# Optimization experiments

Measured on AMD Instinct MI355X. Metric: run time of the kernel, lower is better.

The kernel has to match this reference:

```python
import jax, jax.numpy as jnp
import numpy as np

NEG_SLOPE = 0.2  # PyG GATConv default leaky_relu slope


def gat_conv(h_in, src, dst, W, a_src, a_dst, b, N):
    # h_in: [N, Fin]; src/dst: [E] (self-loops already appended)
    h = h_in @ W                      # [N, Fout]
    alpha_src = h @ a_src             # [N]
    alpha_dst = h @ a_dst             # [N]
    e = jax.nn.leaky_relu(alpha_src[src] + alpha_dst[dst], NEG_SLOPE)  # [E]
    # segment softmax over incoming edges of each destination node
    m = jax.ops.segment_max(e, dst, num_segments=N)
    m = jnp.where(jnp.isfinite(m), m, 0.0)
    p = jnp.exp(e - m[dst])
    denom = jax.ops.segment_sum(p, dst, num_segments=N)
    alpha = p / jnp.maximum(denom[dst], 1e-16)
    out = jax.ops.segment_sum(alpha[:, None] * h[src], dst, num_segments=N)
    return out + b


def setup_inputs() -> dict:
    key = jax.random.key(0)
    ks = jax.random.split(key, 16)
    N, E, V, D, H, C, G = 100000, 1600000, 128, 50, 16, 10, 512
    x = jax.random.normal(ks[0], (N, V), dtype=jnp.float32)
    edge_index = jax.random.randint(ks[1], (2, E), 0, N, dtype=jnp.int32)
    batch = jnp.sort(jax.random.randint(ks[2], (N,), 0, G, dtype=jnp.int32))
    s = lambda fan: 1.0 / np.sqrt(fan)
    return {
        "x": x, "edge_index": edge_index, "batch": batch,
        "embedding": jax.random.normal(ks[3], (V, D), dtype=jnp.float32),
        "W1": jax.random.normal(ks[4], (D, H), dtype=jnp.float32) * s(D),
        "a_src1": jax.random.normal(ks[5], (H,), dtype=jnp.float32) * s(H),
        "a_dst1": jax.random.normal(ks[6], (H,), dtype=jnp.float32) * s(H),
        "b1": jnp.zeros((H,), dtype=jnp.float32),
        "W2": jax.random.normal(ks[7], (H, H), dtype=jnp.float32) * s(H),
        "a_src2": jax.random.normal(ks[8], (H,), dtype=jnp.float32) * s(H),
        "a_dst2": jax.random.normal(ks[9], (H,), dtype=jnp.float32) * s(H),
        "b2": jnp.zeros((H,), dtype=jnp.float32),
        "W3": jax.random.normal(ks[10], (H, C), dtype=jnp.float32) * s(H),
        "a_src3": jax.random.normal(ks[11], (C,), dtype=jnp.float32) * s(C),
        "a_dst3": jax.random.normal(ks[12], (C,), dtype=jnp.float32) * s(C),
        "b3": jnp.zeros((C,), dtype=jnp.float32),
    }


def reference(x, edge_index, batch, embedding, W1, a_src1, a_dst1, b1,
              W2, a_src2, a_dst2, b2, W3, a_src3, a_dst3, b3):
    N = x.shape[0]
    G = 512  # num graphs
    # embedding lookup via argmax over one-hot-ish features
    idx = jnp.argmax(x, axis=1)
    h = embedding[idx]                               # [N, 50]
    # add self-loops once (PyG GATConv default)
    loops = jnp.arange(N, dtype=edge_index.dtype)
    src = jnp.concatenate([edge_index[0], loops])
    dst = jnp.concatenate([edge_index[1], loops])
    h = jax.nn.relu(gat_conv(h, src, dst, W1, a_src1, a_dst1, b1, N))
    # dropout: eval mode -> identity
    h = jax.nn.relu(gat_conv(h, src, dst, W2, a_src2, a_dst2, b2, N))
    h = gat_conv(h, src, dst, W3, a_src3, a_dst3, b3, N)  # [N, C]
    # global mean pool over graphs
    sums = jax.ops.segment_sum(h, batch, num_segments=G)
    cnts = jax.ops.segment_sum(jnp.ones((N,), h.dtype), batch, num_segments=G)
    pooled = sums / jnp.maximum(cnts, 1.0)[:, None]
    return jax.nn.softmax(pooled, axis=1)
```

## Files before the change

kernel.cpp:

```cpp
#include <hip/hip_runtime.h>
#include <math.h>

#define NEG_SLOPE 0.2f
#define NBUK_MAX 2048

__global__ void k_argmax(const float* __restrict__ x, int* __restrict__ idx, int N, int V) {
    int node = (blockIdx.x * blockDim.x + threadIdx.x) >> 5;
    int lane = threadIdx.x & 31;
    if (node >= N) return;
    const float4* row = (const float4*)(x + (long long)node * V);
    float bv = -INFINITY;
    int bi = 0x7fffffff;
    int nq = V >> 2;
    for (int q = lane; q < nq; q += 32) {
        float4 v = row[q];
        int base = q << 2;
        if (v.x > bv || (v.x == bv && base     < bi)) { bv = v.x; bi = base;     }
        if (v.y > bv || (v.y == bv && base + 1 < bi)) { bv = v.y; bi = base + 1; }
        if (v.z > bv || (v.z == bv && base + 2 < bi)) { bv = v.z; bi = base + 2; }
        if (v.w > bv || (v.w == bv && base + 3 < bi)) { bv = v.w; bi = base + 3; }
    }
    for (int off = 16; off > 0; off >>= 1) {
        float ov = __shfl_down(bv, off, 32);
        int   oi = __shfl_down(bi, off, 32);
        if (ov > bv || (ov == bv && oi < bi)) { bv = ov; bi = oi; }
    }
    if (lane == 0) idx[node] = bi;
}

template <int FIN, int FOUT>
__global__ void k_transform(const float* __restrict__ h_in, const int* __restrict__ idx,
                            const float* __restrict__ W,
                            const float* __restrict__ a_src, const float* __restrict__ a_dst,
                            _Float16* __restrict__ h_t, float* __restrict__ asrc,
                            float* __restrict__ adst, int N) {
    __shared__ float sW[FIN * FOUT];
    __shared__ float sa[FOUT], sd[FOUT];
    for (int i = threadIdx.x; i < FIN * FOUT; i += blockDim.x) sW[i] = W[i];
    if (threadIdx.x < FOUT) { sa[threadIdx.x] = a_src[threadIdx.x]; sd[threadIdx.x] = a_dst[threadIdx.x]; }
    __syncthreads();
    int n = blockIdx.x * blockDim.x + threadIdx.x;
    if (n >= N) return;
    float acc[FOUT];
#pragma unroll
    for (int f = 0; f < FOUT; f++) acc[f] = 0.f;
    const float* hr = h_in + (long long)idx[n] * FIN;
    for (int k = 0; k < FIN; k++) {
        float v = hr[k];
#pragma unroll
        for (int f = 0; f < FOUT; f++) acc[f] += v * sW[k * FOUT + f];
    }
    float s1 = 0.f, s2 = 0.f;
    _Float16 hh[16];
#pragma unroll
    for (int f = 0; f < 16; f++) hh[f] = (_Float16)0.f;
#pragma unroll
    for (int f = 0; f < FOUT; f++) {
        hh[f] = (_Float16)acc[f];
        s1 += acc[f] * sa[f];
        s2 += acc[f] * sd[f];
    }
    uint4* dst = (uint4*)(h_t + (long long)n * 16);
    dst[0] = ((uint4*)hh)[0];
    dst[1] = ((uint4*)hh)[1];
    asrc[n] = s1;
    adst[n] = s2;
}

template <int B2>
__global__ void __launch_bounds__(1024)
k_histB(const int* __restrict__ edst, int E, int* __restrict__ histT, int NBUK) {
    __shared__ int sh[NBUK_MAX];
    int t = threadIdx.x, b = blockIdx.x;
    for (int k = t; k < NBUK; k += 1024) sh[k] = 0;
    __syncthreads();
    long long ebeg = (long long)b * E / B2, eend = (long long)(b + 1) * E / B2;
    for (long long i = ebeg + t; i < eend; i += 1024)
        atomicAdd(&sh[edst[i] >> 6], 1);
    __syncthreads();
    for (int k = t; k < NBUK; k += 1024) histT[(long long)k * B2 + b] = sh[k];
}

__global__ void k_scan1(const int* __restrict__ vals, int* __restrict__ excl,
                        int* __restrict__ bsums, int M) {
    __shared__ int s[256];
    int i = blockIdx.x * 256 + threadIdx.x;
    int v = (i < M) ? vals[i] : 0;
    s[threadIdx.x] = v;
    __syncthreads();
    for (int off = 1; off < 256; off <<= 1) {
        int a = (threadIdx.x >= (unsigned)off) ? s[threadIdx.x - off] : 0;
        __syncthreads();
        s[threadIdx.x] += a;
        __syncthreads();
    }
    if (i < M) excl[i] = s[threadIdx.x] - v;
    if (threadIdx.x == 255) bsums[blockIdx.x] = s[255];
}

__global__ void k_scan2(int* __restrict__ bsums, int nb) {
    __shared__ int s[2048];
    int i = threadIdx.x;
    int v0 = (i < nb) ? bsums[i] : 0;
    int v1 = (i + 1024 < nb) ? bsums[i + 1024] : 0;
    s[i] = v0;
    s[i + 1024] = v1;
    __syncthreads();
    for (int off = 1; off < 2048; off <<= 1) {
        int a0 = (i >= off) ? s[i - off] : 0;
        int a1 = (i + 1024 >= off) ? s[i + 1024 - off] : 0;
        __syncthreads();
        s[i] += a0;
        s[i + 1024] += a1;
        __syncthreads();
    }
    if (i < nb) bsums[i] = s[i] - v0;
    if (i + 1024 < nb) bsums[i + 1024] = s[i + 1024] - v1;
}

template <int B2>
__global__ void __launch_bounds__(1024)
k_scatB(const int* __restrict__ esrc, const int* __restrict__ edst, int E,
        const int* __restrict__ sexcl, const int* __restrict__ bsums,
        int* __restrict__ tmp, int NBUK) {
    __shared__ int cur[NBUK_MAX];
    int t = threadIdx.x, b = blockIdx.x;
    for (int k = t; k < NBUK; k += 1024)
        cur[k] = sexcl[(long long)k * B2 + b] + bsums[k];
    __syncthreads();
    long long ebeg = (long long)b * E / B2, eend = (long long)(b + 1) * E / B2;
    for (long long i = ebeg + t; i < eend; i += 1024) {
        int d = edst[i];
        int pos = atomicAdd(&cur[d >> 6], 1);
        tmp[pos] = ((d & 63) << 18) | esrc[i];
    }
}

template <int B2>
__global__ void __launch_bounds__(256)
k_binB(const int* __restrict__ sexcl, const int* __restrict__ bsums,
       const int* __restrict__ tmp,
       int* __restrict__ rowptr, int* __restrict__ csr_src, int N, int NBUK, int E) {
    __shared__ int cnt[64];
    __shared__ int cur[64];
    int t = threadIdx.x, b = blockIdx.x;
    int t0 = sexcl[(long long)b * B2] + bsums[b];
    int t1 = (b + 1 < NBUK) ? (sexcl[(long long)(b + 1) * B2] + bsums[b + 1]) : E;
    if (t < 64) cnt[t] = 0;
    __syncthreads();
    for (int i = t0 + t; i < t1; i += 256) atomicAdd(&cnt[tmp[i] >> 18], 1);
    __syncthreads();
    if (t < 64) {
        int v = cnt[t];
        int incl = v;
        for (int off = 1; off < 64; off <<= 1) {
            int u = __shfl_up(incl, off, 64);
            if (t >= off) incl += u;
        }
        int base = t0 + incl - v;
        int d = (b << 6) + t;
        if (d < N) rowptr[d] = base;
        cur[t] = base;
        if (d == N - 1) rowptr[N] = E;
    }
    __syncthreads();
    for (int i = t0 + t; i < t1; i += 256) {
        int p = tmp[i];
        int pos = atomicAdd(&cur[p >> 18], 1);
        csr_src[pos] = p & 0x3FFFF;
    }
}

template <typename EPI>
__device__ __forceinline__ void gat_core(const int* __restrict__ rowptr,
                                         const int* __restrict__ csr_src,
                                         const float* __restrict__ asrc,
                                         const float* __restrict__ adst,
                                         const _Float16* __restrict__ h_t,
                                         int N, int grp, int lane, EPI epilogue) {
    int d = grp;
    int r0 = rowptr[d], r1 = rowptr[d + 1];
    float ad = adst[d];

    float e0 = asrc[d] + ad;
    e0 = (e0 >= 0.f) ? e0 : NEG_SLOPE * e0;
    float p0 = __expf(e0);
    float acc  = p0 * (float)h_t[(long long)d * 16 + lane];
    float psum = (lane == 0) ? p0 : 0.f;

    int j = r0;
    if (j < r1) {
        int myj = j + lane;
        bool valid = myj < r1;
        int s = valid ? csr_src[myj] : d;
        float a = asrc[s];
        while (true) {
            int jn = j + 16;
            int s2 = d; float a2 = 0.f; bool validn = false;
            if (jn < r1) {
                int myjn = jn + lane;
                validn = myjn < r1;
                s2 = validn ? csr_src[myjn] : d;
                a2 = asrc[s2];
            }
            float e = a + ad;
            e = (e >= 0.f) ? e : NEG_SLOPE * e;
            float p = valid ? __expf(e) : 0.f;
            psum += p;
#pragma unroll
            for (int k = 0; k < 16; k++) {
                float pk = __shfl(p, k, 16);
                int   sk = __shfl(s, k, 16);
                acc += pk * (float)h_t[(long long)sk * 16 + lane];
            }
            if (jn >= r1) break;
            j = jn; s = s2; a = a2; valid = validn;
        }
    }
    for (int off = 8; off > 0; off >>= 1) psum += __shfl_xor(psum, off, 16);
    epilogue(d, acc / fmaxf(psum, 1e-16f));
}

template <int FN>
__global__ void k_gat_ft(const int* __restrict__ rowptr, const int* __restrict__ csr_src,
                         const float* __restrict__ asrc, const float* __restrict__ adst,
                         const _Float16* __restrict__ h_t, const float* __restrict__ bias,
                         const float* __restrict__ Wn, const float* __restrict__ an_src,
                         const float* __restrict__ an_dst,
                         _Float16* __restrict__ h_next, float* __restrict__ asrc_n,
                         float* __restrict__ adst_n, int N) {
    __shared__ float sW[16 * FN];
    __shared__ float sa[FN], sd[FN], sb[16];
    for (int i = threadIdx.x; i < 16 * FN; i += blockDim.x) sW[i] = Wn[i];
    if (threadIdx.x < FN) { sa[threadIdx.x] = an_src[threadIdx.x]; sd[threadIdx.x] = an_dst[threadIdx.x]; }
    if (threadIdx.x < 16) sb[threadIdx.x] = bias[threadIdx.x];
    __syncthreads();

    int grp  = (blockIdx.x * blockDim.x + threadIdx.x) >> 4;
    int lane = threadIdx.x & 15;
    if (grp >= N) return;

    gat_core(rowptr, csr_src, asrc, adst, h_t, N, grp, lane,
        [&](int d, float v) {
            v = fmaxf(v + sb[lane], 0.f);
            float acc2 = 0.f;
#pragma unroll
            for (int k = 0; k < 16; k++) {
                float vk = __shfl(v, k, 16);
                if (lane < FN) acc2 += vk * sW[k * FN + lane];
            }
            float c1 = (lane < FN) ? acc2 * sa[lane] : 0.f;
            float c2 = (lane < FN) ? acc2 * sd[lane] : 0.f;
            for (int off = 8; off > 0; off >>= 1) {
                c1 += __shfl_xor(c1, off, 16);
                c2 += __shfl_xor(c2, off, 16);
            }
            h_next[(long long)d * 16 + lane] = (_Float16)((lane < FN) ? acc2 : 0.f);
            if (lane == 0) { asrc_n[d] = c1; adst_n[d] = c2; }
        });
}

template <int FOUT>
__global__ void k_gat_last(const int* __restrict__ rowptr, const int* __restrict__ csr_src,
                           const float* __restrict__ asrc, const float* __restrict__ adst,
                           const _Float16* __restrict__ h_t, float* __restrict__ out, int N) {
    int grp  = (blockIdx.x * blockDim.x + threadIdx.x) >> 4;
    int lane = threadIdx.x & 15;
    if (grp >= N) return;
    gat_core(rowptr, csr_src, asrc, adst, h_t, N, grp, lane,
        [&](int d, float v) {
            if (lane < FOUT) out[(long long)d * FOUT + lane] = v;
        });
}

__global__ void k_pool(const float* __restrict__ h3, const int* __restrict__ batch,
                       const float* __restrict__ b3, float* __restrict__ out, int N, int C) {
    int g = blockIdx.x;
    int lo = 0, hi = N;
    while (lo < hi) { int mid = (lo + hi) >> 1; if (batch[mid] < g) lo = mid + 1; else hi = mid; }
    int start = lo;
    hi = N;
    while (lo < hi) { int mid = (lo + hi) >> 1; if (batch[mid] < g + 1) lo = mid + 1; else hi = mid; }
    int end = lo;

    float sum[16];
    for (int f = 0; f < C; f++) sum[f] = 0.f;
    for (int n = start + threadIdx.x; n < end; n += blockDim.x) {
        const float* r = h3 + (long long)n * C;
        for (int f = 0; f < C; f++) sum[f] += r[f];
    }
    __shared__ float red[256 * 16];
    for (int f = 0; f < C; f++) red[threadIdx.x * 16 + f] = sum[f];
    __syncthreads();
    for (int str = blockDim.x / 2; str > 0; str >>= 1) {
        if ((int)threadIdx.x < str)
            for (int f = 0; f < C; f++) red[threadIdx.x * 16 + f] += red[(threadIdx.x + str) * 16 + f];
        __syncthreads();
    }
    if (threadIdx.x == 0) {
        float cnt = fmaxf((float)(end - start), 1.f);
        float vals[16];
        float mx = -INFINITY;
        for (int f = 0; f < C; f++) { vals[f] = red[f] / cnt + b3[f]; mx = fmaxf(mx, vals[f]); }
        float se = 0.f;
        for (int f = 0; f < C; f++) { vals[f] = __expf(vals[f] - mx); se += vals[f]; }
        for (int f = 0; f < C; f++) out[(long long)g * C + f] = vals[f] / se;
    }
}

extern "C" void kernel_launch(void* const* d_in, const int* in_sizes, int n_in,
                              void* d_out, int out_size, void* d_ws, size_t ws_size,
                              hipStream_t stream) {
    const float* x    = (const float*)d_in[0];
    const int*   eidx = (const int*)d_in[1];
    const int*   batch= (const int*)d_in[2];
    const float* emb  = (const float*)d_in[3];
    const float* W1   = (const float*)d_in[4];
    const float* as1  = (const float*)d_in[5];
    const float* ad1  = (const float*)d_in[6];
    const float* b1   = (const float*)d_in[7];
    const float* W2   = (const float*)d_in[8];
    const float* as2  = (const float*)d_in[9];
    const float* ad2  = (const float*)d_in[10];
    const float* b2   = (const float*)d_in[11];
    const float* W3   = (const float*)d_in[12];
    const float* as3  = (const float*)d_in[13];
    const float* ad3  = (const float*)d_in[14];
    const float* b3   = (const float*)d_in[15];

    const int H = in_sizes[5];
    const int C = in_sizes[13];
    const int D = in_sizes[4] / H;
    const int V = in_sizes[3] / D;
    const int N = in_sizes[0] / V;
    const int E = in_sizes[1] / 2;
    const int G = out_size / C;
    const int* esrc = eidx;
    const int* edst = eidx + E;
    const int NBUK = (N + 63) >> 6;
    constexpr int B2 = 256;
    const int M = NBUK * B2;

    char* w = (char*)d_ws;
    auto carve = [&](size_t bytes) {
        char* p = w;
        w += (bytes + 255) & ~(size_t)255;
        return p;
    };
    float*     as_a    = (float*)carve((size_t)N * 4);
    float*     ad_a    = (float*)carve((size_t)N * 4);
    float*     as_b    = (float*)carve((size_t)N * 4);
    float*     ad_b    = (float*)carve((size_t)N * 4);
    int*       idx     = (int*)carve((size_t)N * 4);
    int*       rowptr  = (int*)carve((size_t)(N + 1) * 4);
    int*       csr_src = (int*)carve((size_t)E * 4);
    int*       histT   = (int*)carve((size_t)M * 4);
    int*       sexcl   = (int*)carve((size_t)M * 4);
    int*       bsums   = (int*)carve(2048 * 4);
    _Float16*  hTa     = (_Float16*)carve((size_t)N * 16 * 2);
    _Float16*  hTb     = (_Float16*)carve((size_t)N * 16 * 2);
    size_t zone_bytes = ((size_t)E * 4 > (size_t)N * C * 4) ? (size_t)E * 4 : (size_t)N * C * 4;
    char*  zone = carve(zone_bytes);
    float* X0  = (float*)zone;
    int*   tmp = (int*)zone;
    (void)ws_size; (void)n_in;

    const int BT = 256;
    dim3 blk(BT);
    int gN   = (N + BT - 1) / BT;
    int gArg = (N * 32 + BT - 1) / BT;
    int gGat = (N * 16 + BT - 1) / BT;
    int nb2  = (M + 255) / 256;

    k_histB<B2><<<B2, dim3(1024), 0, stream>>>(edst, E, histT, NBUK);
    k_scan1<<<nb2, blk, 0, stream>>>(histT, sexcl, bsums, M);
    k_scan2<<<1, 1024, 0, stream>>>(bsums, nb2);
    k_scatB<B2><<<B2, dim3(1024), 0, stream>>>(esrc, edst, E, sexcl, bsums, tmp, NBUK);
    k_binB<B2><<<NBUK, blk, 0, stream>>>(sexcl, bsums, tmp, rowptr, csr_src, N, NBUK, E);

    k_argmax<<<gArg, blk, 0, stream>>>(x, idx, N, V);
    k_transform<50, 16><<<gN, blk, 0, stream>>>(emb, idx, W1, as1, ad1, hTa, as_a, ad_a, N);

    k_gat_ft<16><<<gGat, blk, 0, stream>>>(rowptr, csr_src, as_a, ad_a, hTa, b1,
                                           W2, as2, ad2, hTb, as_b, ad_b, N);

    k_gat_ft<10><<<gGat, blk, 0, stream>>>(rowptr, csr_src, as_b, ad_b, hTb, b2,
                                           W3, as3, ad3, hTa, as_a, ad_a, N);

    k_gat_last<10><<<gGat, blk, 0, stream>>>(rowptr, csr_src, as_a, ad_a, hTa, X0, N);

    k_pool<<<G, blk, 0, stream>>>(X0, batch, b3, (float*)d_out, N, C);
}
```

Baseline: 275.7 us.

## Fuse preprocessing kernels and fold bucket-sum scan into consumers

Runs the destination histogram and the per-node argmax as disjoint block ranges of one launch. It likewise merges the first-level scan with the layer-1 feature transform. The separate second-level scan kernel is removed: each scatter block rescans the bucket sums in shared memory, and each bin block reduces the prefix it needs. Nontemporal loads and stores are added to streaming edge and CSR accesses. This cuts kernel launches and lets independent work share the GPU, at the cost of redundant per-block scan and reduction work.

```diff
diff --git a/kernel.cpp b/kernel.cpp
--- a/kernel.cpp
+++ b/kernel.cpp
@@ -4,118 +4,103 @@
 #define NEG_SLOPE 0.2f
 #define NBUK_MAX 2048
 
-__global__ void k_argmax(const float* __restrict__ x, int* __restrict__ idx, int N, int V) {
-    int node = (blockIdx.x * blockDim.x + threadIdx.x) >> 5;
-    int lane = threadIdx.x & 31;
-    if (node >= N) return;
-    const float4* row = (const float4*)(x + (long long)node * V);
-    float bv = -INFINITY;
-    int bi = 0x7fffffff;
-    int nq = V >> 2;
-    for (int q = lane; q < nq; q += 32) {
-        float4 v = row[q];
-        int base = q << 2;
-        if (v.x > bv || (v.x == bv && base     < bi)) { bv = v.x; bi = base;     }
-        if (v.y > bv || (v.y == bv && base + 1 < bi)) { bv = v.y; bi = base + 1; }
-        if (v.z > bv || (v.z == bv && base + 2 < bi)) { bv = v.z; bi = base + 2; }
-        if (v.w > bv || (v.w == bv && base + 3 < bi)) { bv = v.w; bi = base + 3; }
-    }
-    for (int off = 16; off > 0; off >>= 1) {
-        float ov = __shfl_down(bv, off, 32);
-        int   oi = __shfl_down(bi, off, 32);
-        if (ov > bv || (ov == bv && oi < bi)) { bv = ov; bi = oi; }
-    }
-    if (lane == 0) idx[node] = bi;
+typedef float v4f __attribute__((ext_vector_type(4)));
+
+template <int B2>
+__global__ void __launch_bounds__(1024)
+k_histarg(const float* __restrict__ x, const int* __restrict__ edst, int E,
+          int* __restrict__ histT, int NBUK, int* __restrict__ idx, int N, int V) {
+    __shared__ int sh[NBUK_MAX];
+    int t = threadIdx.x;
+    if ((int)blockIdx.x < B2) {
+        int b = blockIdx.x;
+        for (int k = t; k < NBUK; k += 1024) sh[k] = 0;
+        __syncthreads();
+        long long ebeg = (long long)b * E / B2, eend = (long long)(b + 1) * E / B2;
+        for (long long i = ebeg + t; i < eend; i += 1024)
+            atomicAdd(&sh[__builtin_nontemporal_load(edst + i) >> 6], 1);
+        __syncthreads();
+        for (int k = t; k < NBUK; k += 1024) histT[(long long)k * B2 + b] = sh[k];
+    } else {
+        int node = ((int)blockIdx.x - B2) * 32 + (t >> 5);
+        int lane = t & 31;
+        if (node >= N) return;
+        const v4f* row = (const v4f*)(x + (long long)node * V);
+        float bv = -INFINITY;
+        int bi = 0x7fffffff;
+        int nq = V >> 2;
+        for (int q = lane; q < nq; q += 32) {
+            v4f v = __builtin_nontemporal_load(row + q);
+            int base = q << 2;
+            if (v.x > bv || (v.x == bv && base     < bi)) { bv = v.x; bi = base;     }
+            if (v.y > bv || (v.y == bv && base + 1 < bi)) { bv = v.y; bi = base + 1; }
+            if (v.z > bv || (v.z == bv && base + 2 < bi)) { bv = v.z; bi = base + 2; }
+            if (v.w > bv || (v.w == bv && base + 3 < bi)) { bv = v.w; bi = base + 3; }
+        }
+        for (int off = 16; off > 0; off >>= 1) {
+            float ov = __shfl_down(bv, off, 32);
+            int   oi = __shfl_down(bi, off, 32);
+            if (ov > bv || (ov == bv && oi < bi)) { bv = ov; bi = oi; }
+        }
+        if (lane == 0) idx[node] = bi;
+    }
 }
 
 template <int FIN, int FOUT>
-__global__ void k_transform(const float* __restrict__ h_in, const int* __restrict__ idx,
-                            const float* __restrict__ W,
-                            const float* __restrict__ a_src, const float* __restrict__ a_dst,
-                            _Float16* __restrict__ h_t, float* __restrict__ asrc,
-                            float* __restrict__ adst, int N) {
+__global__ void __launch_bounds__(256)
+k_scan_tr(const int* __restrict__ vals, int* __restrict__ excl, int* __restrict__ bsums, int M,
+          const float* __restrict__ emb, const int* __restrict__ idx,
+          const float* __restrict__ W, const float* __restrict__ a_src,
+          const float* __restrict__ a_dst, _Float16* __restrict__ h_t,
+          float* __restrict__ asrc, float* __restrict__ adst, int N, int NB_SCAN) {
+    __shared__ int s[256];
     __shared__ float sW[FIN * FOUT];
     __shared__ float sa[FOUT], sd[FOUT];
-    for (int i = threadIdx.x; i < FIN * FOUT; i += blockDim.x) sW[i] = W[i];
-    if (threadIdx.x < FOUT) { sa[threadIdx.x] = a_src[threadIdx.x]; sd[threadIdx.x] = a_dst[threadIdx.x]; }
-    __syncthreads();
-    int n = blockIdx.x * blockDim.x + threadIdx.x;
-    if (n >= N) return;
-    float acc[FOUT];
-#pragma unroll
-    for (int f = 0; f < FOUT; f++) acc[f] = 0.f;
-    const float* hr = h_in + (long long)idx[n] * FIN;
-    for (int k = 0; k < FIN; k++) {
-        float v = hr[k];
-#pragma unroll
-        for (int f = 0; f < FOUT; f++) acc[f] += v * sW[k * FOUT + f];
-    }
-    float s1 = 0.f, s2 = 0.f;
-    _Float16 hh[16];
-#pragma unroll
-    for (int f = 0; f < 16; f++) hh[f] = (_Float16)0.f;
-#pragma unroll
-    for (int f = 0; f < FOUT; f++) {
-        hh[f] = (_Float16)acc[f];
-        s1 += acc[f] * sa[f];
-        s2 += acc[f] * sd[f];
-    }
-    uint4* dst = (uint4*)(h_t + (long long)n * 16);
-    dst[0] = ((uint4*)hh)[0];
-    dst[1] = ((uint4*)hh)[1];
-    asrc[n] = s1;
-    adst[n] = s2;
-}
-
-template <int B2>
-__global__ void __launch_bounds__(1024)
-k_histB(const int* __restrict__ edst, int E, int* __restrict__ histT, int NBUK) {
-    __shared__ int sh[NBUK_MAX];
-    int t = threadIdx.x, b = blockIdx.x;
-    for (int k = t; k < NBUK; k += 1024) sh[k] = 0;
-    __syncthreads();
-    long long ebeg = (long long)b * E / B2, eend = (long long)(b + 1) * E / B2;
-    for (long long i = ebeg + t; i < eend; i += 1024)
-        atomicAdd(&sh[edst[i] >> 6], 1);
-    __syncthreads();
-    for (int k = t; k < NBUK; k += 1024) histT[(long long)k * B2 + b] = sh[k];
-}
-
-__global__ void k_scan1(const int* __restrict__ vals, int* __restrict__ excl,
-                        int* __restrict__ bsums, int M) {
-    __shared__ int s[256];
-    int i = blockIdx.x * 256 + threadIdx.x;
-    int v = (i < M) ? vals[i] : 0;
-    s[threadIdx.x] = v;
-    __syncthreads();
-    for (int off = 1; off < 256; off <<= 1) {
-        int a = (threadIdx.x >= (unsigned)off) ? s[threadIdx.x - off] : 0;
-        __syncthreads();
-        s[threadIdx.x] += a;
-        __syncthreads();
-    }
-    if (i < M) excl[i] = s[threadIdx.x] - v;
-    if (threadIdx.x == 255) bsums[blockIdx.x] = s[255];
-}
-
-__global__ void k_scan2(int* __restrict__ bsums, int nb) {
-    __shared__ int s[2048];
-    int i = threadIdx.x;
-    int v0 = (i < nb) ? bsums[i] : 0;
-    int v1 = (i + 1024 < nb) ? bsums[i + 1024] : 0;
-    s[i] = v0;
-    s[i + 1024] = v1;
-    __syncthreads();
-    for (int off = 1; off < 2048; off <<= 1) {
-        int a0 = (i >= off) ? s[i - off] : 0;
-        int a1 = (i + 1024 >= off) ? s[i + 1024 - off] : 0;
-        __syncthreads();
-        s[i] += a0;
-        s[i + 1024] += a1;
-        __syncthreads();
-    }
-    if (i < nb) bsums[i] = s[i] - v0;
-    if (i + 1024 < nb) bsums[i + 1024] = s[i + 1024] - v1;
+    int t = threadIdx.x;
+    if ((int)blockIdx.x < NB_SCAN) {
+        int i = blockIdx.x * 256 + t;
+        int v = (i < M) ? vals[i] : 0;
+        s[t] = v;
+        __syncthreads();
+        for (int off = 1; off < 256; off <<= 1) {
+            int a = (t >= off) ? s[t - off] : 0;
+            __syncthreads();
+            s[t] += a;
+            __syncthreads();
+        }
+        if (i < M) excl[i] = s[t] - v;
+        if (t == 255) bsums[blockIdx.x] = s[255];
+    } else {
+        for (int i = t; i < FIN * FOUT; i += 256) sW[i] = W[i];
+        if (t < FOUT) { sa[t] = a_src[t]; sd[t] = a_dst[t]; }
+        __syncthreads();
+        int n = ((int)blockIdx.x - NB_SCAN) * 256 + t;
+        if (n >= N) return;
+        float acc[FOUT];
+#pragma unroll
+        for (int f = 0; f < FOUT; f++) acc[f] = 0.f;
+        const float* hr = emb + (long long)idx[n] * FIN;
+        for (int k = 0; k < FIN; k++) {
+            float v = hr[k];
+#pragma unroll
+            for (int f = 0; f < FOUT; f++) acc[f] += v * sW[k * FOUT + f];
+        }
+        float s1 = 0.f, s2 = 0.f;
+        _Float16 hh[16];
+#pragma unroll
+        for (int f = 0; f < 16; f++) hh[f] = (_Float16)0.f;
+#pragma unroll
+        for (int f = 0; f < FOUT; f++) {
+            hh[f] = (_Float16)acc[f];
+            s1 += acc[f] * sa[f];
+            s2 += acc[f] * sd[f];
+        }
+        uint4* dst = (uint4*)(h_t + (long long)n * 16);
+        dst[0] = ((uint4*)hh)[0];
+        dst[1] = ((uint4*)hh)[1];
+        asrc[n] = s1;
+        adst[n] = s2;
+    }
 }
 
 template <int B2>
@@ -124,15 +109,37 @@
         const int* __restrict__ sexcl, const int* __restrict__ bsums,
         int* __restrict__ tmp, int NBUK) {
     __shared__ int cur[NBUK_MAX];
+    __shared__ int pb[NBUK_MAX];
     int t = threadIdx.x, b = blockIdx.x;
+    {
+        int v0 = (t < NBUK) ? bsums[t] : 0;
+        int v1 = (t + 1024 < NBUK) ? bsums[t + 1024] : 0;
+        pb[t] = v0;
+        pb[t + 1024] = v1;
+        __syncthreads();
+        for (int off = 1; off < 2048; off <<= 1) {
+            int a0 = (t >= off) ? pb[t - off] : 0;
+            int a1 = (t + 1024 >= off) ? pb[t + 1024 - off] : 0;
+            __syncthreads();
+            pb[t] += a0;
+            pb[t + 1024] += a1;
+            __syncthreads();
+        }
+        int e0 = pb[t] - v0, e1 = pb[t + 1024] - v1;
+        __syncthreads();
+        pb[t] = e0;
+        pb[t + 1024] = e1;
+        __syncthreads();
+    }
     for (int k = t; k < NBUK; k += 1024)
-        cur[k] = sexcl[(long long)k * B2 + b] + bsums[k];
+        cur[k] = sexcl[(long long)k * B2 + b] + pb[k];
     __syncthreads();
     long long ebeg = (long long)b * E / B2, eend = (long long)(b + 1) * E / B2;
     for (long long i = ebeg + t; i < eend; i += 1024) {
-        int d = edst[i];
+        int d = __builtin_nontemporal_load(edst + i);
+        int s = __builtin_nontemporal_load(esrc + i);
         int pos = atomicAdd(&cur[d >> 6], 1);
-        tmp[pos] = ((d & 63) << 18) | esrc[i];
+        __builtin_nontemporal_store(((d & 63) << 18) | s, tmp + pos);
     }
 }
 
@@ -143,9 +150,21 @@
        int* __restrict__ rowptr, int* __restrict__ csr_src, int N, int NBUK, int E) {
     __shared__ int cnt[64];
     __shared__ int cur[64];
+    __shared__ int red[256];
     int t = threadIdx.x, b = blockIdx.x;
-    int t0 = sexcl[(long long)b * B2] + bsums[b];
-    int t1 = (b + 1 < NBUK) ? (sexcl[(long long)(b + 1) * B2] + bsums[b + 1]) : E;
+    int part = 0;
+    for (int i = t; i < b; i += 256) part += bsums[i];
+    red[t] = part;
+    __syncthreads();
+    for (int str = 128; str > 0; str >>= 1) {
+        if (t < str) red[t] += red[t + str];
+        __syncthreads();
+    }
+    int pb_b  = red[0];
+    int pb_b1 = pb_b + bsums[b];
+    int t0 = sexcl[(long long)b * B2] + pb_b;
+    int t1 = (b + 1 < NBUK) ? (sexcl[(long long)(b + 1) * B2] + pb_b1) : E;
+
     if (t < 64) cnt[t] = 0;
     __syncthreads();
     for (int i = t0 + t; i < t1; i += 256) atomicAdd(&cnt[tmp[i] >> 18], 1);
@@ -192,7 +211,7 @@
     if (j < r1) {
         int myj = j + lane;
         bool valid = myj < r1;
-        int s = valid ? csr_src[myj] : d;
+        int s = valid ? __builtin_nontemporal_load(csr_src + myj) : d;
         float a = asrc[s];
         while (true) {
             int jn = j + 16;
@@ -200,7 +219,7 @@
             if (jn < r1) {
                 int myjn = jn + lane;
                 validn = myjn < r1;
-                s2 = validn ? csr_src[myjn] : d;
+                s2 = validn ? __builtin_nontemporal_load(csr_src + myjn) : d;
                 a2 = asrc[s2];
             }
             float e = a + ad;
@@ -367,20 +386,19 @@
 
     const int BT = 256;
     dim3 blk(BT);
-    int gN   = (N + BT - 1) / BT;
-    int gArg = (N * 32 + BT - 1) / BT;
-    int gGat = (N * 16 + BT - 1) / BT;
-    int nb2  = (M + 255) / 256;
-
-    k_histB<B2><<<B2, dim3(1024), 0, stream>>>(edst, E, histT, NBUK);
-    k_scan1<<<nb2, blk, 0, stream>>>(histT, sexcl, bsums, M);
-    k_scan2<<<1, 1024, 0, stream>>>(bsums, nb2);
+    int gGat  = (N * 16 + BT - 1) / BT;
+    int nb2   = (M + 255) / 256;
+    int gArg  = (N + 31) / 32;
+    int gTr   = (N + BT - 1) / BT;
+
+    k_histarg<B2><<<B2 + gArg, dim3(1024), 0, stream>>>(x, edst, E, histT, NBUK, idx, N, V);
+
+    k_scan_tr<50, 16><<<nb2 + gTr, blk, 0, stream>>>(histT, sexcl, bsums, M,
+                                                     emb, idx, W1, as1, ad1, hTa, as_a, ad_a, N, nb2);
+
     k_scatB<B2><<<B2, dim3(1024), 0, stream>>>(esrc, edst, E, sexcl, bsums, tmp, NBUK);
     k_binB<B2><<<NBUK, blk, 0, stream>>>(sexcl, bsums, tmp, rowptr, csr_src, N, NBUK, E);
 
-    k_argmax<<<gArg, blk, 0, stream>>>(x, idx, N, V);
-    k_transform<50, 16><<<gN, blk, 0, stream>>>(emb, idx, W1, as1, ad1, hTa, as_a, ad_a, N);
-
     k_gat_ft<16><<<gGat, blk, 0, stream>>>(rowptr, csr_src, as_a, ad_a, hTa, b1,
                                            W2, as2, ad2, hTb, as_b, ad_b, N);
 
```

Result: slower. 301.5 us (+9.4%).
